# Kernel tuning notes

Measured on AMD Instinct MI355X. Metric: run time of the kernel, lower is better.

The kernel has to match this reference:

```python
import jax, jax.numpy as jnp
import numpy as np

B = 16384
S = 7
CELL = 1.0 / 7.0   # CELL_SILE
LC = 5.0           # lambda_coord
LN = 0.5           # lambda_noobj


def setup_inputs() -> dict:
    key = jax.random.key(0)
    k1, k2, k3 = jax.random.split(key, 3)
    predictions = jax.random.normal(k1, (B, S, S, 30), dtype=jnp.float32)
    targets = jax.random.uniform(k2, (B, S, S, 30), dtype=jnp.float32)
    # channel 4 is the objectness flag; code requires it to be exactly 0 or 1
    conf = (jax.random.uniform(k3, (B, S, S)) < 0.25).astype(jnp.float32)
    targets = targets.at[..., 4].set(conf)
    return {"predictions": predictions, "targets": targets}


def _box_corners(xy, wh):
    # Faithful to the original in-place bug: x2y2 uses the ALREADY-UPDATED x1y1
    xy1 = xy * CELL - wh * 0.5
    xy2 = xy1 * CELL + wh * 0.5
    return xy1, xy2


def _loss_terms(predictions, targets):
    p = predictions.reshape(-1, 30)   # [N, 30], N = B*S*S
    t = targets.reshape(-1, 30)
    obj = (t[:, 4] == 1.0).astype(p.dtype)
    noobj = (t[:, 4] == 0.0).astype(p.dtype)

    # no-object confidence loss on cols 4 and 9
    noobj_loss = LN * jnp.sum(noobj * (jnp.square(p[:, 4] - t[:, 4]) + jnp.square(p[:, 9] - t[:, 9])))

    # two predicted boxes per cell: cols 0:4 and 5:9 ; wh are sqrt-encoded -> square
    pb = jnp.stack([p[:, 0:4], p[:, 5:9]], axis=1)        # [N, 2, 4]
    pxy1, pxy2 = _box_corners(pb[..., 0:2], jnp.square(pb[..., 2:4]))  # [N,2,2]
    txy1, txy2 = _box_corners(t[:, None, 0:2], jnp.square(t[:, None, 2:4]))  # [N,1,2]

    # torchvision.ops.box_iou math (no clamp on areas, clamp(0) on intersection)
    lt = jnp.maximum(pxy1, txy1)
    rb = jnp.minimum(pxy2, txy2)
    inter = jnp.prod(jnp.clip(rb - lt, 0.0, None), axis=-1)   # [N, 2]
    area_p = jnp.prod(pxy2 - pxy1, axis=-1)                   # [N, 2]
    area_t = jnp.prod(txy2 - txy1, axis=-1)                   # [N, 1]
    iou = inter / (area_p + area_t - inter)                   # [N, 2]

    idx = jnp.argmax(iou, axis=1)                             # responsible box in {0,1}

    cols = idx[:, None] * 5 + jnp.arange(4)[None, :]          # [N, 4]
    cp = jnp.take_along_axis(p, cols, axis=1)
    ct = jnp.take_along_axis(t, cols, axis=1)
    center_loss = LC * jnp.sum(obj * jnp.sum(jnp.square(cp[:, 0:2] - ct[:, 0:2]), axis=1))
    wh_loss = LC * jnp.sum(obj * jnp.sum(jnp.square(cp[:, 2:4] - ct[:, 2:4]), axis=1))

    ccol = (idx * 5 + 4)[:, None]
    conf_loss = LC * jnp.sum(obj * jnp.square(jnp.take_along_axis(p, ccol, axis=1) - jnp.take_along_axis(t, ccol, axis=1))[:, 0])

    kcol = (jnp.argmax(t[:, 10:30], axis=1) + 10)[:, None]
    cls_loss = LC * jnp.sum(obj * jnp.square(jnp.take_along_axis(p, kcol, axis=1) - jnp.take_along_axis(t, kcol, axis=1))[:, 0])

    total = noobj_loss + center_loss + wh_loss + conf_loss + cls_loss
    return cls_loss, conf_loss, center_loss + wh_loss, total


def reference(predictions, targets):
    return _loss_terms(predictions, targets)
```

## Files before the change

kernel.cpp:

```cpp
#include <hip/hip_runtime.h>


constexpr int   BLK   = 64;
constexpr int   TILE  = 64;
constexpr int   NC    = 16384 * 7 * 7;
constexpr int   NTILE = NC / TILE;
constexpr int   GRID  = 3136;
constexpr int   ITERS = NTILE / GRID;
constexpr float CELL  = 1.0f / 7.0f;
constexpr float LC    = 5.0f;
constexpr float LN    = 0.5f;

__device__ inline void gload_lds16(const float4* g, float4* l)
{
    __builtin_amdgcn_global_load_lds(
        (const __attribute__((address_space(1))) void*)g,
        (__attribute__((address_space(3))) void*)l,
        16, 0, 0);
}

__device__ inline void stage_tile(const float* __restrict__ P,
                                  const float* __restrict__ T,
                                  int t, float4* dst, int lane)
{
    const float4* gT = reinterpret_cast<const float4*>(T + (size_t)t * 1920);
    const float4* gP = reinterpret_cast<const float4*>(P + (size_t)t * 1920);
    #pragma unroll
    for (int k = 0; k < 15; ++k) {
        const int idx = k * 64 + lane;
        gload_lds16(idx < 480 ? gT + idx : gP + (idx - 480), dst + idx);
    }
}

__launch_bounds__(BLK, 4)
__global__ void yolo_partial(const float* __restrict__ P, const float* __restrict__ T,
                             float4* __restrict__ ws)
{
    __shared__ float4 s4[1920];
    const int lane = threadIdx.x;

    float a_cls = 0.f, a_conf = 0.f, a_cw = 0.f, a_noobj = 0.f;

    stage_tile(P, T, blockIdx.x, s4, lane);

    #pragma unroll
    for (int it = 0; it < ITERS; ++it) {
        const int cur = it & 1;

        if (it + 1 < ITERS)
            stage_tile(P, T, blockIdx.x + (it + 1) * GRID, s4 + ((it + 1) & 1) * 960, lane);

        if (it + 1 < ITERS) asm volatile("s_waitcnt vmcnt(15)" ::: "memory");
        else                asm volatile("s_waitcnt vmcnt(0)"  ::: "memory");
        __builtin_amdgcn_sched_barrier(0);

        const float* sf  = reinterpret_cast<const float*>(s4 + cur * 960);
        const float* myT = sf + (size_t)lane * 30;
        const float* myP = sf + 1920 + (size_t)lane * 30;
        float tv[30], pv[30];
        #pragma unroll
        for (int j = 0; j < 15; ++j) {
            float2 a = reinterpret_cast<const float2*>(myT)[j];
            tv[2 * j] = a.x; tv[2 * j + 1] = a.y;
            float2 b = reinterpret_cast<const float2*>(myP)[j];
            pv[2 * j] = b.x; pv[2 * j + 1] = b.y;
        }

        float best = tv[10], pk = pv[10];
        #pragma unroll
        for (int k = 11; k < 30; ++k) {
            if (tv[k] > best) { best = tv[k]; pk = pv[k]; }
        }

        const float t4    = tv[4];
        const float obj   = (t4 == 1.0f) ? 1.0f : 0.0f;
        const float noobj = (t4 == 0.0f) ? 1.0f : 0.0f;

        float d4 = pv[4] - t4;
        float d9 = pv[9] - tv[9];
        a_noobj += noobj * (d4 * d4 + d9 * d9);

        float tw2 = tv[2] * tv[2], th2 = tv[3] * tv[3];
        float tx1 = tv[0] * CELL - 0.5f * tw2;
        float tx2 = tx1 * CELL + 0.5f * tw2;
        float ty1 = tv[1] * CELL - 0.5f * th2;
        float ty2 = ty1 * CELL + 0.5f * th2;
        float area_t = (tx2 - tx1) * (ty2 - ty1);

        float iou0, iou1;
        #pragma unroll
        for (int b = 0; b < 2; ++b) {
            float bw2 = pv[5 * b + 2] * pv[5 * b + 2];
            float bh2 = pv[5 * b + 3] * pv[5 * b + 3];
            float px1 = pv[5 * b + 0] * CELL - 0.5f * bw2;
            float px2 = px1 * CELL + 0.5f * bw2;
            float py1 = pv[5 * b + 1] * CELL - 0.5f * bh2;
            float py2 = py1 * CELL + 0.5f * bh2;
            float ltx = fmaxf(px1, tx1), lty = fmaxf(py1, ty1);
            float rbx = fminf(px2, tx2), rby = fminf(py2, ty2);
            float inter = fmaxf(rbx - ltx, 0.0f) * fmaxf(rby - lty, 0.0f);
            float area_p = (px2 - px1) * (py2 - py1);
            float iou = inter / (area_p + area_t - inter);
            if (b == 0) iou0 = iou; else iou1 = iou;
        }
        const bool b1 = (iou1 > iou0);

        float cpx = b1 ? pv[5] : pv[0], ctx = b1 ? tv[5] : tv[0];
        float cpy = b1 ? pv[6] : pv[1], cty = b1 ? tv[6] : tv[1];
        float cpw = b1 ? pv[7] : pv[2], ctw = b1 ? tv[7] : tv[2];
        float cph = b1 ? pv[8] : pv[3], cth = b1 ? tv[8] : tv[3];
        float cpc = b1 ? pv[9] : pv[4], ctc = b1 ? tv[9] : tv[4];

        float dx = cpx - ctx, dy = cpy - cty;
        float dw = cpw - ctw, dh = cph - cth;
        a_cw   += obj * (dx * dx + dy * dy + dw * dw + dh * dh);
        float dc = cpc - ctc;
        a_conf += obj * dc * dc;
        float dk = pk - best;
        a_cls  += obj * dk * dk;

        asm volatile("s_waitcnt lgkmcnt(0)" ::: "memory");
        __builtin_amdgcn_sched_barrier(0);
    }

    float vals[4] = { a_cls, a_conf, a_cw, a_noobj };
    #pragma unroll
    for (int c = 0; c < 4; ++c) {
        #pragma unroll
        for (int off = 32; off > 0; off >>= 1)
            vals[c] += __shfl_down(vals[c], off, 64);
    }
    if (lane == 0)
        ws[blockIdx.x] = make_float4(vals[0], vals[1], vals[2], vals[3]);
}

__launch_bounds__(1024, 1)
__global__ void yolo_reduce(const float4* __restrict__ ws, float* __restrict__ out)
{
    __shared__ float red[4][16];
    const int tid = threadIdx.x;

    float s0 = 0.f, s1 = 0.f, s2 = 0.f, s3 = 0.f;
    for (int b = tid; b < GRID; b += 1024) {
        float4 v = ws[b];
        s0 += v.x; s1 += v.y; s2 += v.z; s3 += v.w;
    }
    float vals[4] = { s0, s1, s2, s3 };
    #pragma unroll
    for (int c = 0; c < 4; ++c) {
        #pragma unroll
        for (int off = 32; off > 0; off >>= 1)
            vals[c] += __shfl_down(vals[c], off, 64);
        if ((tid & 63) == 0) red[c][tid >> 6] = vals[c];
    }
    __syncthreads();
    if (tid == 0) {
        float t0 = 0.f, t1 = 0.f, t2 = 0.f, t3 = 0.f;
        #pragma unroll
        for (int w = 0; w < 16; ++w) {
            t0 += red[0][w]; t1 += red[1][w]; t2 += red[2][w]; t3 += red[3][w];
        }
        out[0] = LC * t0;
        out[1] = LC * t1;
        out[2] = LC * t2;
        out[3] = LN * t3 + LC * (t0 + t1 + t2);
    }
}

extern "C" void kernel_launch(void* const* d_in, const int* in_sizes, int n_in,
                              void* d_out, int out_size, void* d_ws, size_t ws_size,
                              hipStream_t stream) {
    const float* P = (const float*)d_in[0];
    const float* T = (const float*)d_in[1];
    float* out = (float*)d_out;
    float4* ws = (float4*)d_ws;

    yolo_partial<<<GRID, BLK, 0, stream>>>(P, T, ws);
    yolo_reduce<<<1, 1024, 0, stream>>>(ws, out);
}
```

Measured before the change: 208.9 us.

## Replace async global-to-LDS double buffering with register-staged prefetch

Drops the direct global_load_lds double-buffered LDS pipeline. Each tile is now loaded into 15 float4 registers, written to a single LDS buffer, and the next tile's loads are issued before the current tile is computed. This halves LDS use and removes the hand-written waitcnt and sched barriers. It costs 60 extra VGPRs, lowers the launch-bounds occupancy hint from 4 to 3, and leaves the compiler to place the waits. Correctness relies on wave-level ordering, since the single-wave block has no __syncthreads.

```diff
diff --git a/kernel.cpp b/kernel.cpp
--- a/kernel.cpp
+++ b/kernel.cpp
@@ -11,50 +11,47 @@
 constexpr float LC    = 5.0f;
 constexpr float LN    = 0.5f;
 
-__device__ inline void gload_lds16(const float4* g, float4* l)
-{
-    __builtin_amdgcn_global_load_lds(
-        (const __attribute__((address_space(1))) void*)g,
-        (__attribute__((address_space(3))) void*)l,
-        16, 0, 0);
-}
-
-__device__ inline void stage_tile(const float* __restrict__ P,
-                                  const float* __restrict__ T,
-                                  int t, float4* dst, int lane)
-{
-    const float4* gT = reinterpret_cast<const float4*>(T + (size_t)t * 1920);
-    const float4* gP = reinterpret_cast<const float4*>(P + (size_t)t * 1920);
-    #pragma unroll
-    for (int k = 0; k < 15; ++k) {
-        const int idx = k * 64 + lane;
-        gload_lds16(idx < 480 ? gT + idx : gP + (idx - 480), dst + idx);
-    }
-}
-
-__launch_bounds__(BLK, 4)
+__launch_bounds__(BLK, 3)
 __global__ void yolo_partial(const float* __restrict__ P, const float* __restrict__ T,
                              float4* __restrict__ ws)
 {
-    __shared__ float4 s4[1920];
+    __shared__ float4 s4[960];
     const int lane = threadIdx.x;
 
     float a_cls = 0.f, a_conf = 0.f, a_cw = 0.f, a_noobj = 0.f;
 
-    stage_tile(P, T, blockIdx.x, s4, lane);
+    float4 r[15];
+    {
+        const int t = blockIdx.x;
+        const float4* gT = reinterpret_cast<const float4*>(T + (size_t)t * 1920);
+        const float4* gP = reinterpret_cast<const float4*>(P + (size_t)t * 1920);
+        #pragma unroll
+        for (int k = 0; k < 15; ++k) {
+            const int idx = k * 64 + lane;
+            r[k] = (idx < 480) ? gT[idx] : gP[idx - 480];
+        }
+    }
 
     #pragma unroll
     for (int it = 0; it < ITERS; ++it) {
-        const int cur = it & 1;
+        #pragma unroll
+        for (int k = 0; k < 15; ++k)
+            s4[k * 64 + lane] = r[k];
+        asm volatile("" ::: "memory");
 
-        if (it + 1 < ITERS)
-            stage_tile(P, T, blockIdx.x + (it + 1) * GRID, s4 + ((it + 1) & 1) * 960, lane);
+        if (it + 1 < ITERS) {
+            const int t = blockIdx.x + (it + 1) * GRID;
+            const float4* gT = reinterpret_cast<const float4*>(T + (size_t)t * 1920);
+            const float4* gP = reinterpret_cast<const float4*>(P + (size_t)t * 1920);
+            #pragma unroll
+            for (int k = 0; k < 15; ++k) {
+                const int idx = k * 64 + lane;
+                r[k] = (idx < 480) ? gT[idx] : gP[idx - 480];
+            }
+        }
+        asm volatile("" ::: "memory");
 
-        if (it + 1 < ITERS) asm volatile("s_waitcnt vmcnt(15)" ::: "memory");
-        else                asm volatile("s_waitcnt vmcnt(0)"  ::: "memory");
-        __builtin_amdgcn_sched_barrier(0);
-
-        const float* sf  = reinterpret_cast<const float*>(s4 + cur * 960);
+        const float* sf  = reinterpret_cast<const float*>(s4);
         const float* myT = sf + (size_t)lane * 30;
         const float* myP = sf + 1920 + (size_t)lane * 30;
         float tv[30], pv[30];
@@ -119,8 +116,7 @@
         float dk = pk - best;
         a_cls  += obj * dk * dk;
 
-        asm volatile("s_waitcnt lgkmcnt(0)" ::: "memory");
-        __builtin_amdgcn_sched_barrier(0);
+        asm volatile("" ::: "memory");
     }
 
     float vals[4] = { a_cls, a_conf, a_cw, a_noobj };
```

New measurement: 240.5 us. +15.1%, slower.
